# Kernel optimization log

Hardware: AMD Instinct MI355X
Metric: run time of the kernel (lower is better)

## Reference

```python
import jax, jax.numpy as jnp
import numpy as np

N = 4096      # batch_size
D = 256       # projection dim
TEMP = 0.5    # temperature


def setup_inputs() -> dict:
    key = jax.random.key(0)
    k1, k2 = jax.random.split(key)
    return {
        "emb_i": jax.random.normal(k1, (N, D), dtype=jnp.float32),
        "emb_j": jax.random.normal(k2, (N, D), dtype=jnp.float32),
    }


def reference(emb_i, emb_j):
    # L2-normalize rows (F.normalize, dim=1)
    z_i = emb_i / jnp.maximum(jnp.linalg.norm(emb_i, axis=1, keepdims=True), 1e-12)
    z_j = emb_j / jnp.maximum(jnp.linalg.norm(emb_j, axis=1, keepdims=True), 1e-12)
    rep = jnp.concatenate([z_i, z_j], axis=0)            # [2N, D]

    # cosine similarity of unit vectors == dot product -> GEMM instead of O(N^2 D) broadcast
    sim = rep @ rep.T                                    # [2N, 2N]

    # positives: diag(sim, +N) and diag(sim, -N) are both sum(z_i*z_j, axis=1)
    pos_ij = jnp.sum(z_i * z_j, axis=1)                  # [N]
    positives = jnp.concatenate([pos_ij, pos_ij], axis=0)  # [2N]

    # mask keeps exactly the two cross-view blocks (main diagonal lies in same-view blocks)
    idx = jnp.arange(2 * N)
    mask = (idx[:, None] < N) != (idx[None, :] < N)      # [2N, 2N] bool

    nominator = jnp.exp(positives / TEMP)                # [2N]
    denominator = jnp.sum(jnp.where(mask, jnp.exp(sim / TEMP), 0.0), axis=1)  # [2N]

    loss_partial = -jnp.log(nominator / (0.5 * denominator))
    return jnp.sum(loss_partial) / (2 * N)
```

## Files before the change

kernel.cpp:

```cpp
#include <hip/hip_runtime.h>
#include <math.h>

#define NROWS 4096
#define DDIM  256
#define BM 128
#define BN 256
#define LOG2E2 2.8853900817779268f

typedef __attribute__((ext_vector_type(8))) short short8;
typedef __attribute__((ext_vector_type(4))) float f32x4;

__device__ __forceinline__ unsigned short f2bf(float f) {
    unsigned int u = __float_as_uint(f);
    u += 0x7fffu + ((u >> 16) & 1u);
    return (unsigned short)(u >> 16);
}

__device__ __forceinline__ float exp2_fast(float x) {
#if __has_builtin(__builtin_amdgcn_exp2f)
    return __builtin_amdgcn_exp2f(x);
#else
    return exp2f(x);
#endif
}

__global__ __launch_bounds__(256) void normalize_kernel(
    const float* __restrict__ emb_i, const float* __restrict__ emb_j,
    unsigned short* __restrict__ zi, unsigned short* __restrict__ zj,
    float* __restrict__ pos, float* __restrict__ sums )
{
    if (threadIdx.x < 8) sums[blockIdx.x * 8 + threadIdx.x] = 0.0f;

    const int wave = threadIdx.x >> 6;
    const int lane = threadIdx.x & 63;
    const int row  = blockIdx.x * 4 + wave;

    const float4 vi = *((const float4*)(emb_i + (size_t)row * DDIM) + lane);
    const float4 vj = *((const float4*)(emb_j + (size_t)row * DDIM) + lane);

    float ssi = vi.x*vi.x + vi.y*vi.y + vi.z*vi.z + vi.w*vi.w;
    float ssj = vj.x*vj.x + vj.y*vj.y + vj.z*vj.z + vj.w*vj.w;
    #pragma unroll
    for (int m = 1; m < 64; m <<= 1) {
        ssi += __shfl_xor(ssi, m);
        ssj += __shfl_xor(ssj, m);
    }
    const float ri = 1.0f / fmaxf(sqrtf(ssi), 1e-12f);
    const float rj = 1.0f / fmaxf(sqrtf(ssj), 1e-12f);

    const float zix = vi.x*ri, ziy = vi.y*ri, ziz = vi.z*ri, ziw = vi.w*ri;
    const float zjx = vj.x*rj, zjy = vj.y*rj, zjz = vj.z*rj, zjw = vj.w*rj;

    float p = zix*zjx + ziy*zjy + ziz*zjz + ziw*zjw;
    #pragma unroll
    for (int m = 1; m < 64; m <<= 1) p += __shfl_xor(p, m);
    if (lane == 0) pos[row] = p;

    ushort4 oi = { f2bf(zix*LOG2E2), f2bf(ziy*LOG2E2), f2bf(ziz*LOG2E2), f2bf(ziw*LOG2E2) };
    ushort4 oj = { f2bf(zjx), f2bf(zjy), f2bf(zjz), f2bf(zjw) };
    *((ushort4*)(zi + (size_t)row * DDIM) + lane) = oi;
    *((ushort4*)(zj + (size_t)row * DDIM) + lane) = oj;
}

__global__ __launch_bounds__(256, 2) void gemm_fused_kernel(
    const unsigned short* __restrict__ zi, const unsigned short* __restrict__ zj,
    float* __restrict__ rowsum, float* __restrict__ colsum)
{
    const int tid  = threadIdx.x;
    const int lane = tid & 63;
    const int wave = tid >> 6;
    const int g    = lane >> 4;
    const int fr   = lane & 15;
    const int wr   = wave >> 1;
    const int wc   = wave & 1;
    const int bm   = blockIdx.x * BM;
    const int bn   = blockIdx.y * BN;

    f32x4 acc[4][8] = {};

    const unsigned short* pA = zi + (size_t)(bm + wr * 64  + fr) * DDIM + g * 8;
    const unsigned short* pB = zj + (size_t)(bn + wc * 128 + fr) * DDIM + g * 8;

    #pragma unroll
    for (int kk = 0; kk < 8; ++kk) {
        short8 a[4], b[8];
        #pragma unroll
        for (int mi = 0; mi < 4; ++mi)
            a[mi] = *(const short8*)(pA + (size_t)mi * 16 * DDIM + kk * 32);
        #pragma unroll
        for (int ni = 0; ni < 8; ++ni)
            b[ni] = *(const short8*)(pB + (size_t)ni * 16 * DDIM + kk * 32);
        #pragma unroll
        for (int mi = 0; mi < 4; ++mi)
            #pragma unroll
            for (int ni = 0; ni < 8; ++ni)
                acc[mi][ni] = __builtin_amdgcn_mfma_f32_16x16x32_bf16(
                    a[mi], b[ni], acc[mi][ni], 0, 0, 0);
    }

    float rp[4][4];
    float cp[8] = {0.f,0.f,0.f,0.f,0.f,0.f,0.f,0.f};
    #pragma unroll
    for (int mi = 0; mi < 4; ++mi)
        #pragma unroll
        for (int j = 0; j < 4; ++j) rp[mi][j] = 0.f;

    #pragma unroll
    for (int mi = 0; mi < 4; ++mi)
        #pragma unroll
        for (int ni = 0; ni < 8; ++ni)
            #pragma unroll
            for (int j = 0; j < 4; ++j) {
                const float e = exp2_fast(acc[mi][ni][j]);
                rp[mi][j] += e;
                cp[ni]    += e;
            }

    #pragma unroll
    for (int mi = 0; mi < 4; ++mi)
        #pragma unroll
        for (int j = 0; j < 4; ++j) {
            float v = rp[mi][j];
            v += __shfl_xor(v, 1); v += __shfl_xor(v, 2);
            v += __shfl_xor(v, 4); v += __shfl_xor(v, 8);
            if (fr == 0)
                atomicAdd(&rowsum[bm + wr * 64 + mi * 16 + g * 4 + j], v);
        }

    #pragma unroll
    for (int ni = 0; ni < 8; ++ni) {
        float v = cp[ni];
        v += __shfl_xor(v, 16); v += __shfl_xor(v, 32);
        if (g == 0)
            atomicAdd(&colsum[bn + wc * 128 + ni * 16 + fr], v);
    }
}

__global__ __launch_bounds__(512) void finalize_kernel(
    const float* __restrict__ pos, const float* __restrict__ rowsum,
    const float* __restrict__ colsum, float* __restrict__ out)
{
    float s = 0.0f;
    for (int r = threadIdx.x; r < NROWS; r += 512) {
        s += -4.0f * pos[r] + logf(0.25f * rowsum[r] * colsum[r]);
    }
    __shared__ float part[8];
    #pragma unroll
    for (int m = 1; m < 64; m <<= 1) s += __shfl_xor(s, m);
    if ((threadIdx.x & 63) == 0) part[threadIdx.x >> 6] = s;
    __syncthreads();
    if (threadIdx.x == 0) {
        float t = 0.f;
        #pragma unroll
        for (int w = 0; w < 8; ++w) t += part[w];
        out[0] = t / (2.0f * NROWS);
    }
}

extern "C" void kernel_launch(void* const* d_in, const int* in_sizes, int n_in,
                              void* d_out, int out_size, void* d_ws, size_t ws_size,
                              hipStream_t stream)
{
    const float* emb_i = (const float*)d_in[0];
    const float* emb_j = (const float*)d_in[1];

    unsigned short* zi = (unsigned short*)d_ws;
    unsigned short* zj = zi + (size_t)NROWS * DDIM;
    float* pos    = (float*)(zj + (size_t)NROWS * DDIM);
    float* rowsum = pos + NROWS;
    float* colsum = rowsum + NROWS;

    normalize_kernel<<<NROWS / 4, 256, 0, stream>>>(emb_i, emb_j, zi, zj, pos, rowsum);

    dim3 grid(NROWS / BM, NROWS / BN);
    gemm_fused_kernel<<<grid, 256, 0, stream>>>(zi, zj, rowsum, colsum);

    finalize_kernel<<<1, 512, 0, stream>>>(pos, rowsum, colsum, (float*)d_out);
}
```

Before: 93.09 us.

## Stage GEMM operands through double-buffered LDS with direct global-to-LDS loads

Replaces the per-wave direct global loads of A and B fragments with cooperative global_load_lds transfers into swizzled, double-buffered shared-memory tiles, and MFMA operands are then read from LDS. Each K-slice is loaded once per block instead of being re-fetched by multiple waves, and the next slice's load overlaps the current slice's MFMAs. The cost is extra LDS (48 KB per block), which may limit occupancy, plus a barrier per K step.

```diff
diff --git a/kernel.cpp b/kernel.cpp
--- a/kernel.cpp
+++ b/kernel.cpp
@@ -5,6 +5,7 @@
 #define DDIM  256
 #define BM 128
 #define BN 256
+#define BK 32
 #define LOG2E2 2.8853900817779268f
 
 typedef __attribute__((ext_vector_type(8))) short short8;
@@ -24,6 +25,11 @@
 #endif
 }
 
+#define GLOAD_LDS16(gsrc, ldst)                                          \
+    __builtin_amdgcn_global_load_lds(                                    \
+        (__attribute__((address_space(1))) void*)(gsrc),                 \
+        (__attribute__((address_space(3))) void*)(ldst), 16, 0, 0)
+
 __global__ __launch_bounds__(256) void normalize_kernel(
     const float* __restrict__ emb_i, const float* __restrict__ emb_j,
     unsigned short* __restrict__ zi, unsigned short* __restrict__ zj,
@@ -66,6 +72,9 @@
     const unsigned short* __restrict__ zi, const unsigned short* __restrict__ zj,
     float* __restrict__ rowsum, float* __restrict__ colsum)
 {
+    __shared__ unsigned short As[2][BM * BK];
+    __shared__ unsigned short Bs[2][BN * BK];
+
     const int tid  = threadIdx.x;
     const int lane = tid & 63;
     const int wave = tid >> 6;
@@ -78,24 +87,49 @@
 
     f32x4 acc[4][8] = {};
 
-    const unsigned short* pA = zi + (size_t)(bm + wr * 64  + fr) * DDIM + g * 8;
-    const unsigned short* pB = zj + (size_t)(bn + wc * 128 + fr) * DDIM + g * 8;
-
-    #pragma unroll
-    for (int kk = 0; kk < 8; ++kk) {
+    auto stage = [&](int buf, int k0) {
+        #pragma unroll
+        for (int it = 0; it < 2; ++it) {
+            const int L   = it * 256 + tid;
+            const int row = L >> 2;
+            const int sl  = (L & 3) ^ ((row >> 1) & 3);
+            GLOAD_LDS16(zi + (size_t)(bm + row) * DDIM + k0 + sl * 8,
+                        &As[buf][(it * 256 + wave * 64) << 3]);
+        }
+        #pragma unroll
+        for (int it = 0; it < 4; ++it) {
+            const int L   = it * 256 + tid;
+            const int row = L >> 2;
+            const int sl  = (L & 3) ^ ((row >> 1) & 3);
+            GLOAD_LDS16(zj + (size_t)(bn + row) * DDIM + k0 + sl * 8,
+                        &Bs[buf][(it * 256 + wave * 64) << 3]);
+        }
+    };
+
+    auto compute = [&](int buf) {
+        const int coff = ((g ^ ((fr >> 1) & 3)) << 3);
         short8 a[4], b[8];
         #pragma unroll
         for (int mi = 0; mi < 4; ++mi)
-            a[mi] = *(const short8*)(pA + (size_t)mi * 16 * DDIM + kk * 32);
+            a[mi] = *(const short8*)&As[buf][(wr * 64 + mi * 16 + fr) * BK + coff];
         #pragma unroll
         for (int ni = 0; ni < 8; ++ni)
-            b[ni] = *(const short8*)(pB + (size_t)ni * 16 * DDIM + kk * 32);
+            b[ni] = *(const short8*)&Bs[buf][(wc * 128 + ni * 16 + fr) * BK + coff];
         #pragma unroll
         for (int mi = 0; mi < 4; ++mi)
             #pragma unroll
             for (int ni = 0; ni < 8; ++ni)
                 acc[mi][ni] = __builtin_amdgcn_mfma_f32_16x16x32_bf16(
                     a[mi], b[ni], acc[mi][ni], 0, 0, 0);
+    };
+
+    stage(0, 0);
+    __syncthreads();
+    #pragma unroll
+    for (int t = 0; t < 8; ++t) {
+        if (t < 7) stage((t + 1) & 1, (t + 1) * BK);
+        compute(t & 1);
+        if (t < 7) __syncthreads();
     }
 
     float rp[4][4];
```

Measured after the change: 81.24 us. 1.15x faster.
